# Optimization experiments

Measured on AMD Instinct MI355X. Metric: run time of the kernel, lower is better.

## Reference

```python
import jax, jax.numpy as jnp
import numpy as np

EPS = 1e-12  # torch F.normalize default eps

def _l1_normalize(x):
    # F.normalize(x, p=1, dim=1): divide by channel-wise L1 norm, clamped at eps
    n = jnp.sum(jnp.abs(x), axis=1, keepdims=True)
    return x / jnp.maximum(n, EPS)

def setup_inputs() -> dict:
    key = jax.random.key(0)
    k1, k2, k3 = jax.random.split(key, 3)
    shape = (2, 128, 64, 64)  # B, C, H, W
    return {
        "a": jax.random.normal(k1, shape, dtype=jnp.float32),
        "b": jax.random.normal(k2, shape, dtype=jnp.float32),
        "c": jax.random.normal(k3, shape, dtype=jnp.float32),
    }

def reference(a, b, c):
    a = _l1_normalize(a)
    b = _l1_normalize(b)
    c = _l1_normalize(c)
    sim_ab = jnp.einsum('bchw,bcij->bhwij', a, b)
    sim_ac = jnp.einsum('bchw,bcij->bhwij', a, c)
    # F.l1_loss default reduction='mean'
    return jnp.mean(jnp.abs(sim_ac - sim_ab))
```

## Files before the change

### kernel.cpp

```cpp
#include <hip/hip_runtime.h>
#include <stdint.h>

#define HW 4096
#define NC 128
#define BATCH 2

typedef __attribute__((ext_vector_type(8))) short bf16x8;
typedef __attribute__((ext_vector_type(4))) float f32x4;
typedef __attribute__((ext_vector_type(8))) unsigned short u16x8;

__device__ __forceinline__ unsigned short f32_to_bf16(float f) {
    union { float f; unsigned int u; } v; v.f = f;
    unsigned int u = v.u;
    unsigned int r = (u + 0x7FFFu + ((u >> 16) & 1u)) >> 16;
    return (unsigned short)r;
}

__device__ __forceinline__ void async_cp16(const void* g, void* s) {
    __builtin_amdgcn_global_load_lds(
        (const __attribute__((address_space(1))) uint32_t*)g,
        (__attribute__((address_space(3))) uint32_t*)s, 16, 0, 0);
}

__global__ __launch_bounds__(256) void norm_kernel(
    const float* __restrict__ A, const float* __restrict__ B,
    const float* __restrict__ Cc,
    unsigned short* __restrict__ anT, unsigned short* __restrict__ dT,
    float* __restrict__ out) {
    const int tid = threadIdx.x;
    if (blockIdx.x == 0 && tid == 0) *out = 0.f;
    const int pl = tid & 15;
    const int cg = tid >> 4;
    const int gp = blockIdx.x * 32;
    const int bb = gp >> 12;
    const int p0 = (gp & (HW - 1)) + pl * 2;
    const size_t base = (size_t)bb * NC * HW + p0;
    const int c0 = cg * 8;

    float2 va[8], vb[8], vc[8];
    float sa0 = 0.f, sa1 = 0.f, sb0 = 0.f, sb1 = 0.f, sc0 = 0.f, sc1 = 0.f;
#pragma unroll
    for (int k = 0; k < 8; ++k) {
        size_t idx = base + (size_t)(c0 + k) * HW;
        va[k] = *(const float2*)(A + idx);
        vb[k] = *(const float2*)(B + idx);
        vc[k] = *(const float2*)(Cc + idx);
        sa0 += fabsf(va[k].x); sa1 += fabsf(va[k].y);
        sb0 += fabsf(vb[k].x); sb1 += fabsf(vb[k].y);
        sc0 += fabsf(vc[k].x); sc1 += fabsf(vc[k].y);
    }
    __shared__ float red[3][16][32];
    red[0][cg][pl * 2] = sa0; red[0][cg][pl * 2 + 1] = sa1;
    red[1][cg][pl * 2] = sb0; red[1][cg][pl * 2 + 1] = sb1;
    red[2][cg][pl * 2] = sc0; red[2][cg][pl * 2 + 1] = sc1;
    __syncthreads();
    float na0 = 0.f, na1 = 0.f, nb0 = 0.f, nb1 = 0.f, nc0 = 0.f, nc1 = 0.f;
#pragma unroll
    for (int g = 0; g < 16; ++g) {
        na0 += red[0][g][pl * 2]; na1 += red[0][g][pl * 2 + 1];
        nb0 += red[1][g][pl * 2]; nb1 += red[1][g][pl * 2 + 1];
        nc0 += red[2][g][pl * 2]; nc1 += red[2][g][pl * 2 + 1];
    }
    const float ra0 = 1.f / fmaxf(na0, 1e-12f), ra1 = 1.f / fmaxf(na1, 1e-12f);
    const float rb0 = 1.f / fmaxf(nb0, 1e-12f), rb1 = 1.f / fmaxf(nb1, 1e-12f);
    const float rc0 = 1.f / fmaxf(nc0, 1e-12f), rc1 = 1.f / fmaxf(nc1, 1e-12f);

    const size_t ob0 = ((size_t)bb * HW + p0) * NC;
    const size_t ob1 = ob0 + NC;
    const int sl0 = cg ^ (p0 & 15);
    const int sl1 = cg ^ ((p0 + 1) & 15);
    u16x8 xa0, xa1, xd0, xd1;
#pragma unroll
    for (int j = 0; j < 8; ++j) {
        xa0[j] = f32_to_bf16(va[j].x * ra0);
        xa1[j] = f32_to_bf16(va[j].y * ra1);
        xd0[j] = f32_to_bf16(vc[j].x * rc0 - vb[j].x * rb0);
        xd1[j] = f32_to_bf16(vc[j].y * rc1 - vb[j].y * rb1);
    }
    *(u16x8*)(anT + ob0 + sl0 * 8) = xa0;
    *(u16x8*)(anT + ob1 + sl1 * 8) = xa1;
    *(u16x8*)(dT  + ob0 + sl0 * 8) = xd0;
    *(u16x8*)(dT  + ob1 + sl1 * 8) = xd1;
}

__global__ __launch_bounds__(256, 2) void simloss_kernel(
    const unsigned short* __restrict__ anT, const unsigned short* __restrict__ dT,
    float* __restrict__ out) {
    __shared__ uint4 smem4[4096];
    const int tid = threadIdx.x;
    const int b   = blockIdx.x;
    const int bz  = b >> 8;
    const int my  = (b & 255) >> 3;
    const int ng  = b & 7;
    const char* gA  = (const char*)(anT + ((size_t)bz * HW + my * 128) * NC);
    const char* gB0 = (const char*)(dT + ((size_t)bz * HW + ng * 4 * 128) * NC);

    const int wv = tid >> 6;
    const int ln = tid & 63;
    char* buf0 = (char*)smem4;
    char* buf1 = (char*)(smem4 + 2048);

#pragma unroll
    for (int i = 0; i < 8; ++i) {
        const size_t goff = (size_t)(i * 256 + tid) * 16;
        const size_t loff = (size_t)i * 4096 + wv * 1024;
        async_cp16(gA + goff, buf0 + loff);
        async_cp16(gB0 + goff, buf1 + loff);
    }
    __syncthreads();

    const int m16  = ln & 15;
    const int quad = ln >> 4;
    const int wr   = (wv >> 1) * 64;
    const int wc   = (wv & 1) * 64;

    bf16x8 aF[4][4];
#pragma unroll
    for (int ks = 0; ks < 4; ++ks) {
        const int slot = (ks * 4 + quad) ^ m16;
#pragma unroll
        for (int mi = 0; mi < 4; ++mi)
            aF[mi][ks] = *(const bf16x8*)(buf0 + (wr + mi * 16 + m16) * 256 + slot * 16);
    }
    __syncthreads();

#pragma unroll
    for (int i = 0; i < 8; ++i)
        async_cp16(gB0 + 32768 + (size_t)(i * 256 + tid) * 16,
                   buf0 + (size_t)i * 4096 + wv * 1024);

    float s = 0.f;
    for (int j = 0; j < 4; ++j) {
        if (j) {
            __syncthreads();
            if (j < 3) {
                char* dst = (j & 1) ? buf1 : buf0;
                const char* src = gB0 + (size_t)(j + 1) * 32768;
#pragma unroll
                for (int i = 0; i < 8; ++i)
                    async_cp16(src + (size_t)(i * 256 + tid) * 16,
                               dst + (size_t)i * 4096 + wv * 1024);
            }
        }
        const char* sB = (j & 1) ? buf0 : buf1;
        f32x4 acc[4][4] = {};
#pragma unroll
        for (int ks = 0; ks < 4; ++ks) {
            const int slot = (ks * 4 + quad) ^ m16;
            bf16x8 bfr[4];
#pragma unroll
            for (int ni = 0; ni < 4; ++ni)
                bfr[ni] = *(const bf16x8*)(sB + (wc + ni * 16 + m16) * 256 + slot * 16);
#pragma unroll
            for (int mi = 0; mi < 4; ++mi)
#pragma unroll
                for (int ni = 0; ni < 4; ++ni)
                    acc[mi][ni] = __builtin_amdgcn_mfma_f32_16x16x32_bf16(
                        aF[mi][ks], bfr[ni], acc[mi][ni], 0, 0, 0);
        }
#pragma unroll
        for (int mi = 0; mi < 4; ++mi)
#pragma unroll
            for (int ni = 0; ni < 4; ++ni)
#pragma unroll
                for (int r = 0; r < 4; ++r)
                    s += fabsf(acc[mi][ni][r]);
    }

#pragma unroll
    for (int off = 32; off > 0; off >>= 1)
        s += __shfl_down(s, off);
    __syncthreads();
    if (ln == 0) ((float*)smem4)[wv] = s;
    __syncthreads();
    if (tid == 0) {
        const float inv = 1.0f / ((float)BATCH * (float)HW * (float)HW);
        float t = ((float*)smem4)[0] + ((float*)smem4)[1] +
                  ((float*)smem4)[2] + ((float*)smem4)[3];
        atomicAdd(out, t * inv);
    }
}

extern "C" void kernel_launch(void* const* d_in, const int* in_sizes, int n_in,
                              void* d_out, int out_size, void* d_ws, size_t ws_size,
                              hipStream_t stream) {
    const float* A  = (const float*)d_in[0];
    const float* B  = (const float*)d_in[1];
    const float* Cc = (const float*)d_in[2];
    float* out = (float*)d_out;
    unsigned short* anT = (unsigned short*)d_ws;
    unsigned short* dT  = anT + (size_t)BATCH * HW * NC;

    norm_kernel<<<dim3(256), dim3(256), 0, stream>>>(A, B, Cc, anT, dT, out);
    simloss_kernel<<<dim3(512), dim3(256), 0, stream>>>(anT, dT, out);
}
```

Measured before the change: 80.73 us.

## Fuse normalize and similarity-loss kernels with a global grid barrier

```diff
diff --git a/kernel.cpp b/kernel.cpp
--- a/kernel.cpp
+++ b/kernel.cpp
@@ -4,10 +4,13 @@
 #define HW 4096
 #define NC 128
 #define BATCH 2
+#define NBLK 512
 
 typedef __attribute__((ext_vector_type(8))) short bf16x8;
 typedef __attribute__((ext_vector_type(4))) float f32x4;
 typedef __attribute__((ext_vector_type(8))) unsigned short u16x8;
+
+__device__ unsigned long long g_ctr = 0ULL;
 
 __device__ __forceinline__ unsigned short f32_to_bf16(float f) {
     union { float f; unsigned int u; } v; v.f = f;
@@ -22,76 +25,79 @@
         (__attribute__((address_space(3))) uint32_t*)s, 16, 0, 0);
 }
 
-__global__ __launch_bounds__(256) void norm_kernel(
+__global__ __launch_bounds__(256, 2) void fused_kernel(
     const float* __restrict__ A, const float* __restrict__ B,
     const float* __restrict__ Cc,
     unsigned short* __restrict__ anT, unsigned short* __restrict__ dT,
     float* __restrict__ out) {
-    const int tid = threadIdx.x;
-    if (blockIdx.x == 0 && tid == 0) *out = 0.f;
-    const int pl = tid & 15;
-    const int cg = tid >> 4;
-    const int gp = blockIdx.x * 32;
-    const int bb = gp >> 12;
-    const int p0 = (gp & (HW - 1)) + pl * 2;
-    const size_t base = (size_t)bb * NC * HW + p0;
-    const int c0 = cg * 8;
-
-    float2 va[8], vb[8], vc[8];
-    float sa0 = 0.f, sa1 = 0.f, sb0 = 0.f, sb1 = 0.f, sc0 = 0.f, sc1 = 0.f;
-#pragma unroll
-    for (int k = 0; k < 8; ++k) {
-        size_t idx = base + (size_t)(c0 + k) * HW;
-        va[k] = *(const float2*)(A + idx);
-        vb[k] = *(const float2*)(B + idx);
-        vc[k] = *(const float2*)(Cc + idx);
-        sa0 += fabsf(va[k].x); sa1 += fabsf(va[k].y);
-        sb0 += fabsf(vb[k].x); sb1 += fabsf(vb[k].y);
-        sc0 += fabsf(vc[k].x); sc1 += fabsf(vc[k].y);
-    }
-    __shared__ float red[3][16][32];
-    red[0][cg][pl * 2] = sa0; red[0][cg][pl * 2 + 1] = sa1;
-    red[1][cg][pl * 2] = sb0; red[1][cg][pl * 2 + 1] = sb1;
-    red[2][cg][pl * 2] = sc0; red[2][cg][pl * 2 + 1] = sc1;
-    __syncthreads();
-    float na0 = 0.f, na1 = 0.f, nb0 = 0.f, nb1 = 0.f, nc0 = 0.f, nc1 = 0.f;
-#pragma unroll
-    for (int g = 0; g < 16; ++g) {
-        na0 += red[0][g][pl * 2]; na1 += red[0][g][pl * 2 + 1];
-        nb0 += red[1][g][pl * 2]; nb1 += red[1][g][pl * 2 + 1];
-        nc0 += red[2][g][pl * 2]; nc1 += red[2][g][pl * 2 + 1];
-    }
-    const float ra0 = 1.f / fmaxf(na0, 1e-12f), ra1 = 1.f / fmaxf(na1, 1e-12f);
-    const float rb0 = 1.f / fmaxf(nb0, 1e-12f), rb1 = 1.f / fmaxf(nb1, 1e-12f);
-    const float rc0 = 1.f / fmaxf(nc0, 1e-12f), rc1 = 1.f / fmaxf(nc1, 1e-12f);
-
-    const size_t ob0 = ((size_t)bb * HW + p0) * NC;
-    const size_t ob1 = ob0 + NC;
-    const int sl0 = cg ^ (p0 & 15);
-    const int sl1 = cg ^ ((p0 + 1) & 15);
-    u16x8 xa0, xa1, xd0, xd1;
-#pragma unroll
-    for (int j = 0; j < 8; ++j) {
-        xa0[j] = f32_to_bf16(va[j].x * ra0);
-        xa1[j] = f32_to_bf16(va[j].y * ra1);
-        xd0[j] = f32_to_bf16(vc[j].x * rc0 - vb[j].x * rb0);
-        xd1[j] = f32_to_bf16(vc[j].y * rc1 - vb[j].y * rb1);
-    }
-    *(u16x8*)(anT + ob0 + sl0 * 8) = xa0;
-    *(u16x8*)(anT + ob1 + sl1 * 8) = xa1;
-    *(u16x8*)(dT  + ob0 + sl0 * 8) = xd0;
-    *(u16x8*)(dT  + ob1 + sl1 * 8) = xd1;
-}
-
-__global__ __launch_bounds__(256, 2) void simloss_kernel(
-    const unsigned short* __restrict__ anT, const unsigned short* __restrict__ dT,
-    float* __restrict__ out) {
     __shared__ uint4 smem4[4096];
     const int tid = threadIdx.x;
     const int b   = blockIdx.x;
-    const int bz  = b >> 8;
-    const int my  = (b & 255) >> 3;
-    const int ng  = b & 7;
+
+    if (b == 0 && tid == 0) *out = 0.f;
+
+    {
+        const int pl = tid & 15;
+        const int cg = tid >> 4;
+        const int gp = b * 16;
+        const int bb = gp >> 12;
+        const int p  = (gp & (HW - 1)) + pl;
+        const size_t base = (size_t)bb * NC * HW + p;
+        const int c0 = cg * 8;
+
+        float va[8], vb[8], vc[8];
+        float sa = 0.f, sb = 0.f, sc = 0.f;
+#pragma unroll
+        for (int k = 0; k < 8; ++k) {
+            size_t idx = base + (size_t)(c0 + k) * HW;
+            va[k] = A[idx]; vb[k] = B[idx]; vc[k] = Cc[idx];
+            sa += fabsf(va[k]); sb += fabsf(vb[k]); sc += fabsf(vc[k]);
+        }
+        float* red = (float*)smem4;
+        red[(0 * 16 + cg) * 16 + pl] = sa;
+        red[(1 * 16 + cg) * 16 + pl] = sb;
+        red[(2 * 16 + cg) * 16 + pl] = sc;
+        __syncthreads();
+        float na = 0.f, nb = 0.f, nc = 0.f;
+#pragma unroll
+        for (int g = 0; g < 16; ++g) {
+            na += red[(0 * 16 + g) * 16 + pl];
+            nb += red[(1 * 16 + g) * 16 + pl];
+            nc += red[(2 * 16 + g) * 16 + pl];
+        }
+        const float ra = 1.f / fmaxf(na, 1e-12f);
+        const float rb = 1.f / fmaxf(nb, 1e-12f);
+        const float rc = 1.f / fmaxf(nc, 1e-12f);
+
+        const size_t obase = ((size_t)bb * HW + p) * NC;
+        const int slot = cg ^ pl;
+        u16x8 xa, xd;
+#pragma unroll
+        for (int j = 0; j < 8; ++j) {
+            xa[j] = f32_to_bf16(va[j] * ra);
+            xd[j] = f32_to_bf16(vc[j] * rc - vb[j] * rb);
+        }
+        *(u16x8*)(anT + obase + slot * 8) = xa;
+        *(u16x8*)(dT  + obase + slot * 8) = xd;
+    }
+
+    __threadfence();
+    __syncthreads();
+    if (tid == 0) {
+        unsigned long long t = __hip_atomic_fetch_add(
+            &g_ctr, 1ULL, __ATOMIC_ACQ_REL, __HIP_MEMORY_SCOPE_AGENT);
+        unsigned long long target = (t / (unsigned long long)NBLK + 1ULL) *
+                                    (unsigned long long)NBLK;
+        while (__hip_atomic_load(&g_ctr, __ATOMIC_ACQUIRE,
+                                 __HIP_MEMORY_SCOPE_AGENT) < target)
+            __builtin_amdgcn_s_sleep(2);
+    }
+    __syncthreads();
+    __threadfence();
+
+    const int bz = b >> 8;
+    const int my = (b & 255) >> 3;
+    const int ng = b & 7;
     const char* gA  = (const char*)(anT + ((size_t)bz * HW + my * 128) * NC);
     const char* gB0 = (const char*)(dT + ((size_t)bz * HW + ng * 4 * 128) * NC);
 
@@ -191,6 +197,5 @@
     unsigned short* anT = (unsigned short*)d_ws;
     unsigned short* dT  = anT + (size_t)BATCH * HW * NC;
 
-    norm_kernel<<<dim3(256), dim3(256), 0, stream>>>(A, B, Cc, anT, dT, out);
-    simloss_kernel<<<dim3(512), dim3(256), 0, stream>>>(anT, dT, out);
-}
+    fused_kernel<<<dim3(NBLK), dim3(256), 0, stream>>>(A, B, Cc, anT, dT, out);
+}
```

Result: slower. 190.8 us (+136.3%).
